# Kernel optimization log

Hardware: AMD Instinct MI355X
Metric: run time of the kernel (lower is better)

## Reference

```python
import jax, jax.numpy as jnp
import numpy as np

N_NODES = 100000
N_EDGES = 3200000
IN_DIM = 256
UNITS = 128


def setup_inputs() -> dict:
    key = jax.random.key(0)
    k1, k2, k3, k4, k5 = jax.random.split(key, 5)
    x = jax.random.normal(k1, (N_NODES, IN_DIM), dtype=jnp.float32)
    kernel = jax.random.normal(k2, (IN_DIM, UNITS), dtype=jnp.float32) * (1.0 / np.sqrt(IN_DIM))
    adj_rows = jax.random.randint(k3, (N_EDGES,), 0, N_NODES, dtype=jnp.int32)
    adj_cols = jax.random.randint(k4, (N_EDGES,), 0, N_NODES, dtype=jnp.int32)
    adj_vals = jax.random.uniform(k5, (N_EDGES,), dtype=jnp.float32)
    return {"x": x, "kernel": kernel, "adj_rows": adj_rows,
            "adj_cols": adj_cols, "adj_vals": adj_vals}


def reference(x, kernel, adj_rows, adj_cols, adj_vals):
    # Dense transform: [N, in_dim] @ [in_dim, units] -> [N, units]
    h = jnp.matmul(x, kernel)
    # SpMM: out[r] = sum_{edges e with row r} val[e] * h[col[e]]
    msgs = h[adj_cols] * adj_vals[:, None]            # [E, units] gather
    agg = jax.ops.segment_sum(msgs, adj_rows, num_segments=N_NODES)  # scatter-add
    # use_bias=False -> no bias add. Activation: relu.
    return jax.nn.relu(agg)
```

## Files before the change

### kernel.cpp

```cpp
#include <hip/hip_runtime.h>
#include <hip/hip_fp16.h>

#define UNITS 128
#define IN_DIM 256

#define BSHIFT 6
#define BROWS  64
#define NBMAX  1600
#define BCAP   2432
#define BIN_CHUNK 8192

#define GR   64
#define GKC  64
#define APAD 36
#define BPAD 72

typedef short bf16x8 __attribute__((ext_vector_type(8)));
typedef float f32x4  __attribute__((ext_vector_type(4)));
union FragU { uint4 u; bf16x8 f; };

__device__ inline unsigned short bf16_bits(float a) {
  unsigned u = __float_as_uint(a);
  return (unsigned short)((u + 0x7FFF + ((u >> 16) & 1)) >> 16);
}
__device__ inline unsigned pack_bf16x2(float a, float b) {
  return (unsigned)bf16_bits(a) | ((unsigned)bf16_bits(b) << 16);
}

__global__ __launch_bounds__(256) void wt_kernel(
    const float* __restrict__ W, unsigned short* __restrict__ WT) {
  const int i = blockIdx.x * 256 + threadIdx.x;
  const int k = i >> 7;
  const int n = i & 127;
  WT[n * IN_DIM + k] = bf16_bits(W[i]);
}

__global__ __launch_bounds__(256) void fused_gemm_bin_kernel(
    const float* __restrict__ x, const unsigned short* __restrict__ WT,
    __half* __restrict__ h,
    const int* __restrict__ rows, const int* __restrict__ cols,
    const float* __restrict__ vals, int* __restrict__ bcount,
    int2* __restrict__ binned, int n_nodes, int n_edges, int nbuckets) {
  __shared__ __align__(16) char smem[27648];
  const int tid = threadIdx.x;
  const int g = blockIdx.x / 5;
  const int r = blockIdx.x % 5;

  if (r == 4) {
    int* sh_cnt = (int*)smem;
    const int e0    = g * BIN_CHUNK;
    const int e_end = min(e0 + BIN_CHUNK, n_edges);

    for (int i = tid; i < nbuckets; i += 256) sh_cnt[i] = 0;
    __syncthreads();
    for (int e = e0 + tid * 4; e < e_end; e += 1024) {
      const int4 r4 = *(const int4*)(rows + e);
      atomicAdd(&sh_cnt[r4.x >> BSHIFT], 1);
      atomicAdd(&sh_cnt[r4.y >> BSHIFT], 1);
      atomicAdd(&sh_cnt[r4.z >> BSHIFT], 1);
      atomicAdd(&sh_cnt[r4.w >> BSHIFT], 1);
    }
    __syncthreads();
    for (int i = tid; i < nbuckets; i += 256) {
      const int c = sh_cnt[i];
      sh_cnt[i] = c ? atomicAdd(&bcount[i], c) : 0;
    }
    __syncthreads();
    for (int e = e0 + tid * 4; e < e_end; e += 1024) {
      const int4   r4 = *(const int4*)(rows + e);
      const int4   c4 = *(const int4*)(cols + e);
      const float4 v4 = *(const float4*)(vals + e);
#pragma unroll
      for (int u = 0; u < 4; ++u) {
        const int rr = (&r4.x)[u];
        const int cc = (&c4.x)[u];
        const int b  = rr >> BSHIFT;
        const int pos = atomicAdd(&sh_cnt[b], 1);
        if (pos < BCAP)
          binned[(size_t)b * BCAP + pos] = make_int2(
              (int)(((unsigned)(rr & (BROWS - 1)) << 25) | ((unsigned)cc << 8)),
              __float_as_int((&v4.x)[u]));
      }
    }
    return;
  }

  const int gemm_idx = g * 4 + r;
  const int row0 = gemm_idx * GR;
  if (row0 >= n_nodes) return;

  unsigned*       A_lds = (unsigned*)smem;
  unsigned short* B_lds = (unsigned short*)(smem + 9216);

  const int lane = tid & 63;
  const int wave = tid >> 6;
  const int m    = lane & 15;
  const int quad = lane >> 4;

  f32x4 acc[8];
#pragma unroll
  for (int i = 0; i < 8; ++i) acc[i] = (f32x4){0.f, 0.f, 0.f, 0.f};

  for (int k0 = 0; k0 < IN_DIM; k0 += GKC) {
#pragma unroll
    for (int p = 0; p < 4; ++p) {
      const int idx = tid + p * 256;
      const int rr  = idx >> 4;
      const int c4  = idx & 15;
      const int gr  = row0 + rr;
      float4 v = make_float4(0.f, 0.f, 0.f, 0.f);
      if (gr < n_nodes)
        v = *(const float4*)(x + (size_t)gr * IN_DIM + k0 + c4 * 4);
      unsigned* dst = &A_lds[rr * APAD + c4 * 2];
      dst[0] = pack_bf16x2(v.x, v.y);
      dst[1] = pack_bf16x2(v.z, v.w);
    }
#pragma unroll
    for (int p = 0; p < 4; ++p) {
      const int u = tid + p * 256;
      const int n = u >> 3;
      const int c = u & 7;
      const uint4 v = *(const uint4*)(WT + (size_t)n * IN_DIM + k0 + c * 8);
      *(uint4*)&B_lds[n * BPAD + c * 8] = v;
    }
    __syncthreads();

#pragma unroll
    for (int ks = 0; ks < 2; ++ks) {
      FragU a;
      a.u = *(const uint4*)&A_lds[(wave * 16 + m) * APAD + ks * 16 + quad * 4];
#pragma unroll
      for (int nt = 0; nt < 8; ++nt) {
        FragU b;
        b.u = *(const uint4*)&B_lds[(nt * 16 + m) * BPAD + ks * 32 + quad * 8];
        acc[nt] = __builtin_amdgcn_mfma_f32_16x16x32_bf16(a.f, b.f, acc[nt], 0, 0, 0);
      }
    }
    __syncthreads();
  }

  const int orow = row0 + wave * 16 + quad * 4;
#pragma unroll
  for (int nt = 0; nt < 8; ++nt) {
    const int col = nt * 16 + m;
#pragma unroll
    for (int i = 0; i < 4; ++i) {
      const int rr = orow + i;
      if (rr < n_nodes)
        h[(size_t)rr * UNITS + col] = __float2half(acc[nt][i]);
    }
  }
}

#define SA_TPB 512

__global__ __launch_bounds__(SA_TPB) void sortagg_kernel(
    const int* __restrict__ bcount, const int2* __restrict__ binned,
    const __half* __restrict__ h, float* __restrict__ out, int n_nodes) {
  __shared__ int2 sedge[BCAP];
  __shared__ int  shist[BROWS];
  __shared__ int  sstart[BROWS + 1];
  __shared__ int  scur[BROWS];

  const int tid  = threadIdx.x;
  const int lane = tid & 63;
  const int wv   = tid >> 6;
  const int b    = blockIdx.x;
  const int row0 = b << BSHIFT;

  int cnt = bcount[b]; if (cnt > BCAP) cnt = BCAP;

  int2 my[5];
#pragma unroll
  for (int k = 0; k < 5; ++k) {
    const int j = tid + k * SA_TPB;
    my[k] = (j < cnt) ? binned[(size_t)b * BCAP + j] : make_int2(0, 0);
  }

  if (tid < BROWS) shist[tid] = 0;
  __syncthreads();
#pragma unroll
  for (int k = 0; k < 5; ++k) {
    const int j = tid + k * SA_TPB;
    if (j < cnt) atomicAdd(&shist[(unsigned)my[k].x >> 25], 1);
  }
  __syncthreads();

  if (wv == 0) {
    const int orig = shist[lane];
    int v = orig;
#pragma unroll
    for (int off = 1; off < 64; off <<= 1) {
      const int u = __shfl_up(v, off, 64);
      if (lane >= off) v += u;
    }
    sstart[lane] = v - orig;
    scur[lane]   = v - orig;
    if (lane == 63) sstart[64] = v;
  }
  __syncthreads();

#pragma unroll
  for (int k = 0; k < 5; ++k) {
    const int j = tid + k * SA_TPB;
    if (j < cnt) {
      const int rl  = (unsigned)my[k].x >> 25;
      const int pos = atomicAdd(&scur[rl], 1);
      sedge[pos] = make_int2(my[k].x & 0x01FFFF00, my[k].y);
    }
  }
  __syncthreads();

  const char* hb = (const char*)h + (lane << 2);
#pragma unroll 1
  for (int i = 0; i < 8; ++i) {
    const int rl  = wv * 8 + i;
    const int row = row0 + rl;
    if (row >= n_nodes) break;
    const int e0 = sstart[rl];
    const int e1 = sstart[rl + 1];
    float accx = 0.f, accy = 0.f;
    for (int j = e0; j < e1; j += 8) {
      float v[8]; float2 f[8];
#pragma unroll
      for (int u = 0; u < 8; ++u) {
        const int idx = j + u;
        const int2 q = sedge[idx < e1 ? idx : e0];
        v[u] = (idx < e1) ? __int_as_float(q.y) : 0.f;
        f[u] = __half22float2(*(const __half2*)(hb + (unsigned)q.x));
      }
#pragma unroll
      for (int u = 0; u < 8; ++u) {
        accx = fmaf(v[u], f[u].x, accx);
        accy = fmaf(v[u], f[u].y, accy);
      }
    }
    float2 o;
    o.x = accx > 0.f ? accx : 0.f;
    o.y = accy > 0.f ? accy : 0.f;
    ((float2*)(out + (size_t)row * UNITS))[lane] = o;
  }
}

extern "C" void kernel_launch(void* const* d_in, const int* in_sizes, int n_in,
                              void* d_out, int out_size, void* d_ws, size_t ws_size,
                              hipStream_t stream) {
  const float* x     = (const float*)d_in[0];
  const float* W     = (const float*)d_in[1];
  const int*   rows  = (const int*)d_in[2];
  const int*   cols  = (const int*)d_in[3];
  const float* vals  = (const float*)d_in[4];
  float*       out   = (float*)d_out;

  const int n_nodes = in_sizes[0] / IN_DIM;
  const int n_edges = in_sizes[2];
  const int nbuckets = (n_nodes + BROWS - 1) >> BSHIFT;

  char* ws = (char*)d_ws;
  size_t off = 0;
  auto alloc = [&](size_t bytes) {
    char* p = ws + off;
    off += (bytes + 511) & ~(size_t)511;
    return p;
  };
  __half*         h      = (__half*)alloc((size_t)n_nodes * UNITS * sizeof(__half));
  unsigned short* WT     = (unsigned short*)alloc((size_t)UNITS * IN_DIM * 2);
  int*            bcount = (int*)   alloc((size_t)nbuckets * sizeof(int));
  int2*           binned = (int2*)  alloc((size_t)nbuckets * BCAP * sizeof(int2));

  wt_kernel<<<(IN_DIM * UNITS) / 256, 256, 0, stream>>>(W, WT);
  hipMemsetAsync(bcount, 0, (size_t)nbuckets * sizeof(int), stream);

  const int nbin = (n_edges + BIN_CHUNK - 1) / BIN_CHUNK;
  fused_gemm_bin_kernel<<<nbin * 5, 256, 0, stream>>>(
      x, WT, h, rows, cols, vals, bcount, binned, n_nodes, n_edges, nbuckets);

  sortagg_kernel<<<nbuckets, SA_TPB, 0, stream>>>(bcount, binned, h, out, n_nodes);
}
```

Measured before the change: 376.9 us.

## Interleave binning and GEMM per block; pad per-row edge lists to drop bounds checks

The fused kernel no longer splits blocks into separate GEMM and binning roles. Every 512-thread block now computes a 128-row GEMM tile and also bins a 4096-edge slice, with the order alternating between even and odd blocks so memory-bound and compute-bound phases overlap across the GPU. In the aggregation kernel, each row's edge list is padded to a multiple of 8 with zeroed entries. This removes the per-element bounds selects in the gather loop, and the kernel now uses 256 threads per block, with each wave handling 16 rows. The costs are a shared-memory zero-fill and a slightly smaller per-bucket capacity, which could drop edges if a bucket overflows.

```diff
diff --git a/kernel.cpp b/kernel.cpp
--- a/kernel.cpp
+++ b/kernel.cpp
@@ -7,10 +7,11 @@
 #define BSHIFT 6
 #define BROWS  64
 #define NBMAX  1600
-#define BCAP   2432
-#define BIN_CHUNK 8192
-
-#define GR   64
+#define BCAP   2368
+#define SEDGE  2816
+#define BIN_SLICE 4096
+
+#define GR   128
 #define GKC  64
 #define APAD 36
 #define BPAD 72
@@ -35,38 +36,38 @@
   WT[n * IN_DIM + k] = bf16_bits(W[i]);
 }
 
-__global__ __launch_bounds__(256) void fused_gemm_bin_kernel(
-    const float* __restrict__ x, const unsigned short* __restrict__ WT,
-    __half* __restrict__ h,
+__device__ __forceinline__ void do_bin(
+    int* sh_cnt, int bid,
     const int* __restrict__ rows, const int* __restrict__ cols,
     const float* __restrict__ vals, int* __restrict__ bcount,
-    int2* __restrict__ binned, int n_nodes, int n_edges, int nbuckets) {
-  __shared__ __align__(16) char smem[27648];
+    int2* __restrict__ binned, int n_edges, int nbuckets) {
   const int tid = threadIdx.x;
-  const int g = blockIdx.x / 5;
-  const int r = blockIdx.x % 5;
-
-  if (r == 4) {
-    int* sh_cnt = (int*)smem;
-    const int e0    = g * BIN_CHUNK;
-    const int e_end = min(e0 + BIN_CHUNK, n_edges);
-
-    for (int i = tid; i < nbuckets; i += 256) sh_cnt[i] = 0;
-    __syncthreads();
-    for (int e = e0 + tid * 4; e < e_end; e += 1024) {
+  const int e0 = bid * BIN_SLICE;
+  const int e_end = min(e0 + BIN_SLICE, n_edges);
+
+  for (int i = tid; i < nbuckets; i += 512) sh_cnt[i] = 0;
+  __syncthreads();
+#pragma unroll
+  for (int p = 0; p < 2; ++p) {
+    const int e = e0 + (tid + p * 512) * 4;
+    if (e < e_end) {
       const int4 r4 = *(const int4*)(rows + e);
       atomicAdd(&sh_cnt[r4.x >> BSHIFT], 1);
       atomicAdd(&sh_cnt[r4.y >> BSHIFT], 1);
       atomicAdd(&sh_cnt[r4.z >> BSHIFT], 1);
       atomicAdd(&sh_cnt[r4.w >> BSHIFT], 1);
     }
-    __syncthreads();
-    for (int i = tid; i < nbuckets; i += 256) {
-      const int c = sh_cnt[i];
-      sh_cnt[i] = c ? atomicAdd(&bcount[i], c) : 0;
-    }
-    __syncthreads();
-    for (int e = e0 + tid * 4; e < e_end; e += 1024) {
+  }
+  __syncthreads();
+  for (int i = tid; i < nbuckets; i += 512) {
+    const int c = sh_cnt[i];
+    sh_cnt[i] = c ? atomicAdd(&bcount[i], c) : 0;
+  }
+  __syncthreads();
+#pragma unroll
+  for (int p = 0; p < 2; ++p) {
+    const int e = e0 + (tid + p * 512) * 4;
+    if (e < e_end) {
       const int4   r4 = *(const int4*)(rows + e);
       const int4   c4 = *(const int4*)(cols + e);
       const float4 v4 = *(const float4*)(vals + e);
@@ -82,18 +83,21 @@
               __float_as_int((&v4.x)[u]));
       }
     }
-    return;
-  }
-
-  const int gemm_idx = g * 4 + r;
-  const int row0 = gemm_idx * GR;
-  if (row0 >= n_nodes) return;
-
+  }
+  __syncthreads();
+}
+
+__device__ __forceinline__ void do_gemm(
+    char* smem, int bid,
+    const float* __restrict__ x, const unsigned short* __restrict__ WT,
+    __half* __restrict__ h, int n_nodes) {
   unsigned*       A_lds = (unsigned*)smem;
-  unsigned short* B_lds = (unsigned short*)(smem + 9216);
-
+  unsigned short* B_lds = (unsigned short*)(smem + 18432);
+
+  const int tid  = threadIdx.x;
   const int lane = tid & 63;
   const int wave = tid >> 6;
+  const int row0 = bid * GR;
   const int m    = lane & 15;
   const int quad = lane >> 4;
 
@@ -104,7 +108,7 @@
   for (int k0 = 0; k0 < IN_DIM; k0 += GKC) {
 #pragma unroll
     for (int p = 0; p < 4; ++p) {
-      const int idx = tid + p * 256;
+      const int idx = tid + p * 512;
       const int rr  = idx >> 4;
       const int c4  = idx & 15;
       const int gr  = row0 + rr;
@@ -116,8 +120,8 @@
       dst[1] = pack_bf16x2(v.z, v.w);
     }
 #pragma unroll
-    for (int p = 0; p < 4; ++p) {
-      const int u = tid + p * 256;
+    for (int p = 0; p < 2; ++p) {
+      const int u = tid + p * 512;
       const int n = u >> 3;
       const int c = u & 7;
       const uint4 v = *(const uint4*)(WT + (size_t)n * IN_DIM + k0 + c * 8);
@@ -152,12 +156,29 @@
   }
 }
 
-#define SA_TPB 512
+__global__ __launch_bounds__(512) void fused_gemm_bin_kernel(
+    const float* __restrict__ x, const unsigned short* __restrict__ WT,
+    __half* __restrict__ h,
+    const int* __restrict__ rows, const int* __restrict__ cols,
+    const float* __restrict__ vals, int* __restrict__ bcount,
+    int2* __restrict__ binned, int n_nodes, int n_edges, int nbuckets) {
+  __shared__ __align__(16) char smem[36864];
+  const int bid = blockIdx.x;
+  const bool bin_first = (bid & 1) == 0;
+
+  if (bin_first)
+    do_bin((int*)smem, bid, rows, cols, vals, bcount, binned, n_edges, nbuckets);
+  do_gemm(smem, bid, x, WT, h, n_nodes);
+  if (!bin_first)
+    do_bin((int*)smem, bid, rows, cols, vals, bcount, binned, n_edges, nbuckets);
+}
+
+#define SA_TPB 256
 
 __global__ __launch_bounds__(SA_TPB) void sortagg_kernel(
     const int* __restrict__ bcount, const int2* __restrict__ binned,
     const __half* __restrict__ h, float* __restrict__ out, int n_nodes) {
-  __shared__ int2 sedge[BCAP];
+  __shared__ int2 sedge[SEDGE];
   __shared__ int  shist[BROWS];
   __shared__ int  sstart[BROWS + 1];
   __shared__ int  scur[BROWS];
@@ -170,17 +191,23 @@
 
   int cnt = bcount[b]; if (cnt > BCAP) cnt = BCAP;
 
-  int2 my[5];
-#pragma unroll
-  for (int k = 0; k < 5; ++k) {
+  int2 my[10];
+#pragma unroll
+  for (int k = 0; k < 10; ++k) {
     const int j = tid + k * SA_TPB;
     my[k] = (j < cnt) ? binned[(size_t)b * BCAP + j] : make_int2(0, 0);
   }
 
+#pragma unroll
+  for (int k = 0; k < 11; ++k) {
+    const int i = tid + k * SA_TPB;
+    if (i < SEDGE) sedge[i] = make_int2(0, 0);
+  }
   if (tid < BROWS) shist[tid] = 0;
   __syncthreads();
-#pragma unroll
-  for (int k = 0; k < 5; ++k) {
+
+#pragma unroll
+  for (int k = 0; k < 10; ++k) {
     const int j = tid + k * SA_TPB;
     if (j < cnt) atomicAdd(&shist[(unsigned)my[k].x >> 25], 1);
   }
@@ -188,20 +215,21 @@
 
   if (wv == 0) {
     const int orig = shist[lane];
-    int v = orig;
+    const int pad  = (orig + 7) & ~7;
+    int v = pad;
 #pragma unroll
     for (int off = 1; off < 64; off <<= 1) {
       const int u = __shfl_up(v, off, 64);
       if (lane >= off) v += u;
     }
-    sstart[lane] = v - orig;
-    scur[lane]   = v - orig;
+    sstart[lane] = v - pad;
+    scur[lane]   = v - pad;
     if (lane == 63) sstart[64] = v;
   }
   __syncthreads();
 
 #pragma unroll
-  for (int k = 0; k < 5; ++k) {
+  for (int k = 0; k < 10; ++k) {
     const int j = tid + k * SA_TPB;
     if (j < cnt) {
       const int rl  = (unsigned)my[k].x >> 25;
@@ -213,20 +241,19 @@
 
   const char* hb = (const char*)h + (lane << 2);
 #pragma unroll 1
-  for (int i = 0; i < 8; ++i) {
-    const int rl  = wv * 8 + i;
+  for (int i = 0; i < 16; ++i) {
+    const int rl  = wv * 16 + i;
     const int row = row0 + rl;
     if (row >= n_nodes) break;
-    const int e0 = sstart[rl];
-    const int e1 = sstart[rl + 1];
+    const int s = sstart[rl];
+    const int e = sstart[rl + 1];
     float accx = 0.f, accy = 0.f;
-    for (int j = e0; j < e1; j += 8) {
+    for (int j = s; j < e; j += 8) {
       float v[8]; float2 f[8];
 #pragma unroll
       for (int u = 0; u < 8; ++u) {
-        const int idx = j + u;
-        const int2 q = sedge[idx < e1 ? idx : e0];
-        v[u] = (idx < e1) ? __int_as_float(q.y) : 0.f;
+        const int2 q = sedge[j + u];
+        v[u] = __int_as_float(q.y);
         f[u] = __half22float2(*(const __half2*)(hb + (unsigned)q.x));
       }
 #pragma unroll
@@ -271,8 +298,8 @@
   wt_kernel<<<(IN_DIM * UNITS) / 256, 256, 0, stream>>>(W, WT);
   hipMemsetAsync(bcount, 0, (size_t)nbuckets * sizeof(int), stream);
 
-  const int nbin = (n_edges + BIN_CHUNK - 1) / BIN_CHUNK;
-  fused_gemm_bin_kernel<<<nbin * 5, 256, 0, stream>>>(
+  const int nblocks = (n_nodes + GR - 1) / GR;
+  fused_gemm_bin_kernel<<<nblocks, 512, 0, stream>>>(
       x, WT, h, rows, cols, vals, bcount, binned, n_nodes, n_edges, nbuckets);
 
   sortagg_kernel<<<nbuckets, SA_TPB, 0, stream>>>(bcount, binned, h, out, n_nodes);
```

After: 379.0 us. No clear change (+0.6%).
